# Optimization experiments

Hardware: AMD Instinct MI355X
Metric: run time of the kernel (lower is better)

## Reference

```python
import jax, jax.numpy as jnp
import numpy as np

NUM_CLUSTERS = 56
HEIGHT = 224
WIDTH = 224
BATCH = 32
FEAT_C = 64


def setup_inputs() -> dict:
    key = jax.random.key(0)
    combined_features = jax.random.normal(key, (BATCH, FEAT_C + 1, HEIGHT, WIDTH), dtype=jnp.float32)
    # std parameter init: num_clusters / sqrt(H*W)
    std = jnp.asarray(NUM_CLUSTERS / (HEIGHT * WIDTH) ** 0.5, dtype=jnp.float32)
    return {"combined_features": combined_features, "std": std}


def _sobel(edges):
    # edges: [B,1,H,W], 3x3 sobel with padding=1 (fixed, non-learnable filters)
    kx = jnp.array([[-1., 0., 1.], [-2., 0., 2.], [-1., 0., 1.]], jnp.float32)[None, None]
    ky = jnp.array([[-1., -2., -1.], [0., 0., 0.], [1., 2., 1.]], jnp.float32)[None, None]
    conv = lambda k: jax.lax.conv_general_dilated(edges, k, (1, 1), [(1, 1), (1, 1)])
    return conv(kx), conv(ky)


def reference(combined_features, std):
    B, Cp1, H, W = combined_features.shape
    K = NUM_CLUSTERS
    edges = combined_features[:, -1:]      # [B,1,H,W]
    features = combined_features[:, :-1]   # [B,C,H,W]

    # --- centroid seeding from edge map ---
    Gx, Gy = _sobel(edges)
    grad_mag = jnp.sqrt(Gx ** 2 + Gy ** 2)
    inverted = 1.0 - 0.5 * grad_mag                      # [B,1,H,W]
    # adaptive_avg_pool2d to (K,K); H,W divisible by K -> exact reshape-mean
    pooled = inverted[:, 0].reshape(B, K, H // K, K, W // K).mean(axis=(2, 4))  # [B,K,K]
    flat = pooled.reshape(B, K * K)
    _, idx = jax.lax.top_k(flat, K)                      # [B,K]
    sy = (idx // K).astype(jnp.float32) / K              # [B,K] in [0,1)
    sx = (idx % K).astype(jnp.float32) / K

    # --- spatial gaussian distance: separable over y and x ---
    y = (jnp.arange(H, dtype=jnp.float32) / H)[None, None, :, None]  # [1,1,H,1]
    x = (jnp.arange(W, dtype=jnp.float32) / W)[None, None, None, :]  # [1,1,1,W]
    dy = y - sy[:, :, None, None]                        # [B,K,H,1]
    dx = x - sx[:, :, None, None]                        # [B,K,1,W]
    # gauss2d(a,b,std) = (exp(-(a/std)^2) + exp(-(b/std)^2)) / 2
    spatial = (jnp.exp(-(dy / std) ** 2) + jnp.exp(-(dx / std) ** 2)) * 0.5  # [B,K,H,W]

    # --- feature distance of each pixel to global mean feature (eps=1e-6 as in F.pairwise_distance) ---
    centroid = features.mean(axis=(2, 3))                # [B,C]
    fdist = jnp.sqrt(jnp.sum((features - centroid[:, :, None, None] + 1e-6) ** 2, axis=1))  # [B,H,W]

    combined = spatial + fdist[:, None]                  # [B,K,H,W]
    markers = jax.nn.softmax(combined, axis=1)           # softmax over clusters
    return markers
```

## Files before the change

kernel.cpp:

```cpp
#include <hip/hip_runtime.h>
#include <math.h>

#define NCLUS 56
#define HH 224
#define WW 224
#define BB 32
#define CELLS (NCLUS * NCLUS)
#define HW (HH * WW)

typedef float f32x4 __attribute__((ext_vector_type(4)));

__global__ __launch_bounds__(256) void pool_kernel(const float* __restrict__ cf,
                                                   float* __restrict__ pooled) {
    __shared__ float lds[18][226];
    int b = blockIdx.x / 14;
    int grp = blockIdx.x - b * 14;
    int tid = threadIdx.x;
    const float* e = cf + ((size_t)b * 65 + 64) * HW;

    int y0 = grp * 16 - 1;
    for (int t = tid; t < 18 * 224; t += 256) {
        int r = t / 224;
        int c = t - r * 224;
        int y = y0 + r;
        lds[r][c + 1] = (y >= 0 && y < HH) ? e[y * WW + c] : 0.0f;
    }
    if (tid < 18) { lds[tid][0] = 0.0f; lds[tid][225] = 0.0f; }
    __syncthreads();

    if (tid >= 224) return;
    int lby = tid / 56;
    int bx = tid - lby * 56;
    int r0 = lby * 4;
    int c0 = bx * 4;

    float patch[6][6];
#pragma unroll
    for (int i = 0; i < 6; ++i)
#pragma unroll
        for (int j = 0; j < 6; ++j) patch[i][j] = lds[r0 + i][c0 + j];

    float s = 0.0f;
#pragma unroll
    for (int iy = 0; iy < 4; ++iy) {
#pragma unroll
        for (int ix = 0; ix < 4; ++ix) {
            float gx = (patch[iy][ix + 2] - patch[iy][ix])
                     + 2.0f * (patch[iy + 1][ix + 2] - patch[iy + 1][ix])
                     + (patch[iy + 2][ix + 2] - patch[iy + 2][ix]);
            float gy = (patch[iy + 2][ix] - patch[iy][ix])
                     + 2.0f * (patch[iy + 2][ix + 1] - patch[iy][ix + 1])
                     + (patch[iy + 2][ix + 2] - patch[iy][ix + 2]);
            float gm = sqrtf(gx * gx + gy * gy);
            s += 1.0f - 0.5f * gm;
        }
    }
    pooled[b * CELLS + (grp * 4 + lby) * NCLUS + bx] = s * 0.0625f;
}

__global__ __launch_bounds__(256) void topk_kernel(
        const float* __restrict__ pooled,
        float* __restrict__ sy, float* __restrict__ sx) {
    int b = blockIdx.x;
    int tid = threadIdx.x;
    __shared__ unsigned long long list[CELLS];
    __shared__ unsigned nlist_s;
    if (tid == 0) nlist_s = 0;

    if (tid < 64) {
        unsigned hi[49];
#pragma unroll
        for (int j = 0; j < 49; ++j) {
            int i = j * 64 + tid;
            unsigned u = __float_as_uint(pooled[b * CELLS + i]);
            hi[j] = (u & 0x80000000u) ? ~u : (u | 0x80000000u);
        }
        unsigned prefix = 0;
        unsigned cnt = CELLS;
        for (int bit = 31; bit >= 0; --bit) {
            if (cnt <= 448u) break;
            unsigned cand = prefix | (1u << bit);
            unsigned c = 0;
#pragma unroll
            for (int j = 0; j < 49; ++j) c += (hi[j] >= cand) ? 1u : 0u;
#pragma unroll
            for (int off = 32; off >= 1; off >>= 1)
                c += __shfl_xor(c, off, 64);
            if (c >= (unsigned)NCLUS) { prefix = cand; cnt = c; }
        }
#pragma unroll
        for (int j = 0; j < 49; ++j) {
            if (hi[j] >= prefix) {
                unsigned pos = atomicAdd(&nlist_s, 1u);
                unsigned i = (unsigned)(j * 64 + tid);
                list[pos] = ((unsigned long long)hi[j] << 32) |
                            (unsigned long long)(0xFFFFFFFFu - i);
            }
        }
    }
    __syncthreads();

    int N = (int)nlist_s;
    for (int c = tid; c < N; c += 256) {
        unsigned long long key = list[c];
        int r = 0;
        for (int j = 0; j < N; ++j) r += (list[j] > key) ? 1 : 0;
        if (r < NCLUS) {
            unsigned idx = 0xFFFFFFFFu - (unsigned)(key & 0xFFFFFFFFull);
            sy[b * NCLUS + r] = (float)(idx / NCLUS) / (float)NCLUS;
            sx[b * NCLUS + r] = (float)(idx % NCLUS) / (float)NCLUS;
        }
    }
}

__global__ __launch_bounds__(448) void markers_kernel(
        const float* __restrict__ sy, const float* __restrict__ sx,
        const float* __restrict__ stdp, float* __restrict__ out) {
    __shared__ float fx_lds[NCLUS][WW];
    __shared__ float fy_s[8 * NCLUS];
    int blk = blockIdx.x;
    int b = blk / 28;
    int h0 = (blk - b * 28) * 8;
    int tid = threadIdx.x;
    float inv_std = 1.0f / stdp[0];
    const float* syb = sy + b * NCLUS;
    const float* sxb = sx + b * NCLUS;

    for (int t = tid; t < NCLUS * WW; t += 448) {
        int k = t / WW;
        int w = t - k * WW;
        float tx = ((float)w / 224.0f - sxb[k]) * inv_std;
        fx_lds[k][w] = expf(0.5f * expf(-(tx * tx)));
    }
    {
        int row = tid / NCLUS;
        int k = tid - row * NCLUS;
        float ty = ((float)(h0 + row) / 224.0f - syb[k]) * inv_std;
        fy_s[tid] = expf(0.5f * expf(-(ty * ty)));
    }
    __syncthreads();

    int row = tid / 56;
    int wq = tid - row * 56;
    const float* fyp = fy_s + row * NCLUS;

    float s0 = 0.f, s1 = 0.f, s2 = 0.f, s3 = 0.f;
#pragma unroll 8
    for (int k = 0; k < NCLUS; ++k) {
        float fy = fyp[k];
        f32x4 fx = *(const f32x4*)&fx_lds[k][wq * 4];
        s0 = fmaf(fy, fx.x, s0);
        s1 = fmaf(fy, fx.y, s1);
        s2 = fmaf(fy, fx.z, s2);
        s3 = fmaf(fy, fx.w, s3);
    }
    float r0 = 1.0f / s0, r1 = 1.0f / s1, r2 = 1.0f / s2, r3 = 1.0f / s3;

    float* op = out + (size_t)b * NCLUS * HW + (size_t)(h0 + row) * WW + wq * 4;
#pragma unroll 8
    for (int k = 0; k < NCLUS; ++k) {
        float fy = fyp[k];
        f32x4 fx = *(const f32x4*)&fx_lds[k][wq * 4];
        f32x4 o;
        o.x = (fy * fx.x) * r0;
        o.y = (fy * fx.y) * r1;
        o.z = (fy * fx.z) * r2;
        o.w = (fy * fx.w) * r3;
        __builtin_nontemporal_store(o, (f32x4*)op);
        op += HW;
    }
}

extern "C" void kernel_launch(void* const* d_in, const int* in_sizes, int n_in,
                              void* d_out, int out_size, void* d_ws,
                              size_t ws_size, hipStream_t stream) {
    const float* cf = (const float*)d_in[0];
    const float* stdp = (const float*)d_in[1];
    float* out = (float*)d_out;

    char* ws = (char*)d_ws;
    float* pooled = (float*)ws;
    float* sy = (float*)(ws + 512 * 1024);
    float* sx = (float*)(ws + 576 * 1024);

    pool_kernel<<<BB * 14, 256, 0, stream>>>(cf, pooled);
    topk_kernel<<<BB, 256, 0, stream>>>(pooled, sy, sx);
    markers_kernel<<<BB * 28, 448, 0, stream>>>(sy, sx, stdp, out);
}
```

Measured before the change: 99.14 us.

## Split markers into normalizer pass and per-cluster contiguous scale-and-store pass

The fused markers kernel is split in two. The first kernel computes only the per-pixel reciprocal softmax denominators into a workspace buffer. The second kernel runs one block per (batch, cluster) and writes a contiguous HxW plane of the output, reading the reciprocal map back. This replaces the strided per-cluster stores, which jumped HW apart, with fully contiguous streaming writes. The cost is an extra launch, a write and re-read of a 6.4MB normalizer buffer, and dropping the nontemporal store hint.

```diff
diff --git a/kernel.cpp b/kernel.cpp
--- a/kernel.cpp
+++ b/kernel.cpp
@@ -113,9 +113,9 @@
     }
 }
 
-__global__ __launch_bounds__(448) void markers_kernel(
+__global__ __launch_bounds__(448) void sums_kernel(
         const float* __restrict__ sy, const float* __restrict__ sx,
-        const float* __restrict__ stdp, float* __restrict__ out) {
+        const float* __restrict__ stdp, float* __restrict__ Sinv) {
     __shared__ float fx_lds[NCLUS][WW];
     __shared__ float fy_s[8 * NCLUS];
     int blk = blockIdx.x;
@@ -154,20 +154,53 @@
         s2 = fmaf(fy, fx.z, s2);
         s3 = fmaf(fy, fx.w, s3);
     }
-    float r0 = 1.0f / s0, r1 = 1.0f / s1, r2 = 1.0f / s2, r3 = 1.0f / s3;
-
-    float* op = out + (size_t)b * NCLUS * HW + (size_t)(h0 + row) * WW + wq * 4;
-#pragma unroll 8
-    for (int k = 0; k < NCLUS; ++k) {
-        float fy = fyp[k];
-        f32x4 fx = *(const f32x4*)&fx_lds[k][wq * 4];
+    f32x4 r;
+    r.x = 1.0f / s0;
+    r.y = 1.0f / s1;
+    r.z = 1.0f / s2;
+    r.w = 1.0f / s3;
+    *(f32x4*)(Sinv + (size_t)b * HW + (size_t)(h0 + row) * WW + wq * 4) = r;
+}
+
+__global__ __launch_bounds__(256) void scale_kernel(
+        const float* __restrict__ sy, const float* __restrict__ sx,
+        const float* __restrict__ stdp, const float* __restrict__ Sinv,
+        float* __restrict__ out) {
+    __shared__ float fy_l[HH];
+    __shared__ float fx_l[WW];
+    int blk = blockIdx.x;
+    int b = blk / NCLUS;
+    int k = blk - b * NCLUS;
+    int tid = threadIdx.x;
+    float inv_std = 1.0f / stdp[0];
+    float syk = sy[b * NCLUS + k];
+    float sxk = sx[b * NCLUS + k];
+
+    for (int t = tid; t < HH; t += 256) {
+        float c = (float)t / 224.0f;
+        float ty = (c - syk) * inv_std;
+        float tx = (c - sxk) * inv_std;
+        fy_l[t] = expf(0.5f * expf(-(ty * ty)));
+        fx_l[t] = expf(0.5f * expf(-(tx * tx)));
+    }
+    __syncthreads();
+
+    const f32x4* sp = (const f32x4*)(Sinv + (size_t)b * HW);
+    f32x4* op = (f32x4*)(out + ((size_t)b * NCLUS + k) * HW);
+#pragma unroll 7
+    for (int i = 0; i < 49; ++i) {
+        int e = i * 256 + tid;
+        int h = e / 56;
+        int w4 = e - h * 56;
+        f32x4 sv = sp[e];
+        float fy = fy_l[h];
+        f32x4 fx = *(const f32x4*)&fx_l[w4 * 4];
         f32x4 o;
-        o.x = (fy * fx.x) * r0;
-        o.y = (fy * fx.y) * r1;
-        o.z = (fy * fx.z) * r2;
-        o.w = (fy * fx.w) * r3;
-        __builtin_nontemporal_store(o, (f32x4*)op);
-        op += HW;
+        o.x = fy * fx.x * sv.x;
+        o.y = fy * fx.y * sv.y;
+        o.z = fy * fx.z * sv.z;
+        o.w = fy * fx.w * sv.w;
+        op[e] = o;
     }
 }
 
@@ -182,8 +215,10 @@
     float* pooled = (float*)ws;
     float* sy = (float*)(ws + 512 * 1024);
     float* sx = (float*)(ws + 576 * 1024);
+    float* Sinv = (float*)(ws + 1024 * 1024);
 
     pool_kernel<<<BB * 14, 256, 0, stream>>>(cf, pooled);
     topk_kernel<<<BB, 256, 0, stream>>>(pooled, sy, sx);
-    markers_kernel<<<BB * 28, 448, 0, stream>>>(sy, sx, stdp, out);
-}
+    sums_kernel<<<BB * 28, 448, 0, stream>>>(sy, sx, stdp, Sinv);
+    scale_kernel<<<BB * NCLUS, 256, 0, stream>>>(sy, sx, stdp, Sinv, out);
+}
```

Result: slower. 127.7 us (+28.8%).

## Precompute per-batch exp tables in topk kernel; load them in markers kernel

Applied to the files above, without the earlier changes.

Moves the double-exp Gaussian factor tables (Fx per cluster/column, Fy per row/cluster) out of the markers kernel into the top-k kernel, which writes them to workspace once per batch. The markers kernel now just copies the tables into LDS. Its grid drops from 896 to 512 blocks, each covering 14 rows over two passes, so the table fill is amortised over more rows. The price is fewer blocks for the store-bound kernel and a longer serial topk kernel running only 32 blocks.

```diff
diff --git a/kernel.cpp b/kernel.cpp
--- a/kernel.cpp
+++ b/kernel.cpp
@@ -58,12 +58,13 @@
     pooled[b * CELLS + (grp * 4 + lby) * NCLUS + bx] = s * 0.0625f;
 }
 
-__global__ __launch_bounds__(256) void topk_kernel(
-        const float* __restrict__ pooled,
-        float* __restrict__ sy, float* __restrict__ sx) {
+__global__ __launch_bounds__(256) void topk_tables_kernel(
+        const float* __restrict__ pooled, const float* __restrict__ stdp,
+        float* __restrict__ Fx, float* __restrict__ Fy) {
     int b = blockIdx.x;
     int tid = threadIdx.x;
     __shared__ unsigned long long list[CELLS];
+    __shared__ float sy_s[NCLUS], sx_s[NCLUS];
     __shared__ unsigned nlist_s;
     if (tid == 0) nlist_s = 0;
 
@@ -107,67 +108,80 @@
         for (int j = 0; j < N; ++j) r += (list[j] > key) ? 1 : 0;
         if (r < NCLUS) {
             unsigned idx = 0xFFFFFFFFu - (unsigned)(key & 0xFFFFFFFFull);
-            sy[b * NCLUS + r] = (float)(idx / NCLUS) / (float)NCLUS;
-            sx[b * NCLUS + r] = (float)(idx % NCLUS) / (float)NCLUS;
-        }
-    }
-}
-
-__global__ __launch_bounds__(448) void markers_kernel(
-        const float* __restrict__ sy, const float* __restrict__ sx,
-        const float* __restrict__ stdp, float* __restrict__ out) {
-    __shared__ float fx_lds[NCLUS][WW];
-    __shared__ float fy_s[8 * NCLUS];
-    int blk = blockIdx.x;
-    int b = blk / 28;
-    int h0 = (blk - b * 28) * 8;
-    int tid = threadIdx.x;
+            sy_s[r] = (float)(idx / NCLUS) / (float)NCLUS;
+            sx_s[r] = (float)(idx % NCLUS) / (float)NCLUS;
+        }
+    }
+    __syncthreads();
+
     float inv_std = 1.0f / stdp[0];
-    const float* syb = sy + b * NCLUS;
-    const float* sxb = sx + b * NCLUS;
-
-    for (int t = tid; t < NCLUS * WW; t += 448) {
+    for (int t = tid; t < NCLUS * WW; t += 256) {
         int k = t / WW;
         int w = t - k * WW;
-        float tx = ((float)w / 224.0f - sxb[k]) * inv_std;
-        fx_lds[k][w] = expf(0.5f * expf(-(tx * tx)));
-    }
-    {
-        int row = tid / NCLUS;
-        int k = tid - row * NCLUS;
-        float ty = ((float)(h0 + row) / 224.0f - syb[k]) * inv_std;
-        fy_s[tid] = expf(0.5f * expf(-(ty * ty)));
-    }
-    __syncthreads();
-
-    int row = tid / 56;
-    int wq = tid - row * 56;
-    const float* fyp = fy_s + row * NCLUS;
-
-    float s0 = 0.f, s1 = 0.f, s2 = 0.f, s3 = 0.f;
+        float tx = ((float)w / 224.0f - sx_s[k]) * inv_std;
+        Fx[(size_t)b * NCLUS * WW + t] = expf(0.5f * expf(-(tx * tx)));
+    }
+    for (int t = tid; t < HH * NCLUS; t += 256) {
+        int h = t / NCLUS;
+        int k = t - h * NCLUS;
+        float ty = ((float)h / 224.0f - sy_s[k]) * inv_std;
+        Fy[(size_t)b * HH * NCLUS + t] = expf(0.5f * expf(-(ty * ty)));
+    }
+}
+
+__global__ __launch_bounds__(448) void markers_kernel(
+        const float* __restrict__ Fx, const float* __restrict__ Fy,
+        float* __restrict__ out) {
+    __shared__ float fx_lds[NCLUS][WW];
+    __shared__ float fy_s[14 * NCLUS];
+    int blk = blockIdx.x;
+    int b = blk / 16;
+    int h0 = (blk - b * 16) * 14;
+    int tid = threadIdx.x;
+
+    const f32x4* fxg = (const f32x4*)(Fx + (size_t)b * NCLUS * WW);
+    f32x4* fxl = (f32x4*)&fx_lds[0][0];
+    for (int t = tid; t < NCLUS * WW / 4; t += 448) fxl[t] = fxg[t];
+    const float* fyg = Fy + ((size_t)b * HH + h0) * NCLUS;
+    for (int t = tid; t < 14 * NCLUS; t += 448) fy_s[t] = fyg[t];
+    __syncthreads();
+
+#pragma unroll
+    for (int q = 0; q < 2; ++q) {
+        int e = q * 448 + tid;
+        if (e < 14 * 56) {
+            int row = e / 56;
+            int wq = e - row * 56;
+            const float* fyp = fy_s + row * NCLUS;
+
+            float s0 = 0.f, s1 = 0.f, s2 = 0.f, s3 = 0.f;
 #pragma unroll 8
-    for (int k = 0; k < NCLUS; ++k) {
-        float fy = fyp[k];
-        f32x4 fx = *(const f32x4*)&fx_lds[k][wq * 4];
-        s0 = fmaf(fy, fx.x, s0);
-        s1 = fmaf(fy, fx.y, s1);
-        s2 = fmaf(fy, fx.z, s2);
-        s3 = fmaf(fy, fx.w, s3);
-    }
-    float r0 = 1.0f / s0, r1 = 1.0f / s1, r2 = 1.0f / s2, r3 = 1.0f / s3;
-
-    float* op = out + (size_t)b * NCLUS * HW + (size_t)(h0 + row) * WW + wq * 4;
+            for (int k = 0; k < NCLUS; ++k) {
+                float fy = fyp[k];
+                f32x4 fx = *(const f32x4*)&fx_lds[k][wq * 4];
+                s0 = fmaf(fy, fx.x, s0);
+                s1 = fmaf(fy, fx.y, s1);
+                s2 = fmaf(fy, fx.z, s2);
+                s3 = fmaf(fy, fx.w, s3);
+            }
+            float r0 = 1.0f / s0, r1 = 1.0f / s1, r2 = 1.0f / s2,
+                  r3 = 1.0f / s3;
+
+            float* op = out + (size_t)b * NCLUS * HW +
+                        (size_t)(h0 + row) * WW + wq * 4;
 #pragma unroll 8
-    for (int k = 0; k < NCLUS; ++k) {
-        float fy = fyp[k];
-        f32x4 fx = *(const f32x4*)&fx_lds[k][wq * 4];
-        f32x4 o;
-        o.x = (fy * fx.x) * r0;
-        o.y = (fy * fx.y) * r1;
-        o.z = (fy * fx.z) * r2;
-        o.w = (fy * fx.w) * r3;
-        __builtin_nontemporal_store(o, (f32x4*)op);
-        op += HW;
+            for (int k = 0; k < NCLUS; ++k) {
+                float fy = fyp[k];
+                f32x4 fx = *(const f32x4*)&fx_lds[k][wq * 4];
+                f32x4 o;
+                o.x = (fy * fx.x) * r0;
+                o.y = (fy * fx.y) * r1;
+                o.z = (fy * fx.z) * r2;
+                o.w = (fy * fx.w) * r3;
+                __builtin_nontemporal_store(o, (f32x4*)op);
+                op += HW;
+            }
+        }
     }
 }
 
@@ -180,10 +194,10 @@
 
     char* ws = (char*)d_ws;
     float* pooled = (float*)ws;
-    float* sy = (float*)(ws + 512 * 1024);
-    float* sx = (float*)(ws + 576 * 1024);
+    float* Fx = (float*)(ws + 512 * 1024);
+    float* Fy = (float*)(ws + 512 * 1024 + 2 * 1024 * 1024);
 
     pool_kernel<<<BB * 14, 256, 0, stream>>>(cf, pooled);
-    topk_kernel<<<BB, 256, 0, stream>>>(pooled, sy, sx);
-    markers_kernel<<<BB * 28, 448, 0, stream>>>(sy, sx, stdp, out);
-}
+    topk_tables_kernel<<<BB, 256, 0, stream>>>(pooled, stdp, Fx, Fy);
+    markers_kernel<<<512, 448, 0, stream>>>(Fx, Fy, out);
+}
```

Result: slower. 113.9 us (+14.9%).
